# Performance work log

Measured on AMD Instinct MI355X. Metric: run time of the kernel, lower is better.

## Reference

```python
import jax, jax.numpy as jnp
import numpy as np

DIM = 16
N_LAYERS = 3
L = 10
CONST = 1.0
SQRT_XI = 1.0  # np.sqrt(xi) with xi=1
BATCH = 1048576

_TRIL = np.array([(k1, k2) for k1 in range(DIM) for k2 in range(k1)], dtype=np.int32)


def _build_M(Q):
    # scatter Q into strict lower triangle, then symmetrize: M^T + M
    M = jnp.zeros((DIM, DIM), Q.dtype).at[_TRIL[:, 0], _TRIL[:, 1]].set(Q)
    return M.T + M


def setup_inputs() -> dict:
    key = jax.random.key(0)
    k1, k2, k3, k4 = jax.random.split(key, 4)
    return {
        "inputs": jnp.zeros((BATCH, 1), jnp.float32),  # only batch size is used
        "Q": jax.random.uniform(k1, (DIM * (DIM - 1) // 2,), jnp.float32, -0.01, 0.01),
        "delta": jax.random.uniform(k2, (DIM,), jnp.float32, -1.0, 1.0),
        "y0": jax.random.normal(k3, (BATCH, DIM), jnp.float32),
        "vel_noise": jax.random.normal(k4, (N_LAYERS, BATCH, DIM), jnp.float32),
    }


def reference(inputs, Q, delta, y0, vel_noise):
    M = _build_M(Q)

    def force(x):  # gradient of tanh-relaxed Ising energy
        return CONST * (delta + x @ M) * (1.0 - jnp.square(x))

    def leap_step(carry, _):
        y, x, vel = carry
        vel_half = vel + 0.5 * SQRT_XI * force(x)
        y = y + SQRT_XI * vel_half
        x = jnp.tanh(CONST * y)
        vel = vel_half + 0.5 * SQRT_XI * force(x)
        return (y, x, vel), None

    def layer_step(carry, vel0):
        y, x = carry
        (y, x, _), _ = jax.lax.scan(leap_step, (y, x, vel0), None, length=L)
        return (y, x), None

    y = y0
    x = jnp.tanh(CONST * y)
    (y, x), _ = jax.lax.scan(layer_step, (y, x), vel_noise)

    # straight-through estimator: forward = sign (0 -> -1), grad = d tanh
    z = CONST * y
    t = jnp.tanh(z)
    hard = jnp.sign(jnp.sign(z) - 1e-6)
    x_out = jax.lax.stop_gradient(hard - t) + t

    energy = jnp.sum(0.5 * (x_out @ M) * x_out + delta * x_out, axis=-1)
    return x_out, energy
```

## Files before the change

kernel.cpp:

```cpp
#include <hip/hip_runtime.h>
#include <math.h>
#include <stdint.h>

#define DIM 16
#define N_LAYERS 3
#define LSTEPS 10

__global__ void build_M_kernel(const float* __restrict__ Q, float* __restrict__ M) {
    int t = threadIdx.x;
    if (t < DIM * DIM) {
        int i = t >> 4, j = t & (DIM - 1);
        float v = 0.0f;
        if (i != j) {
            int a = i > j ? i : j;
            int c = i > j ? j : i;
            v = Q[(a * (a - 1)) / 2 + c];
        }
        M[t] = v;
    }
}

__device__ __forceinline__ float xla_tanh(float x) {
    #pragma clang fp contract(off)
    float xc = fmaxf(fminf(x, 7.99881172180175781f), -7.99881172180175781f);
    float x2 = xc * xc;
    float p = fmaf(x2, -2.76076847742355e-16f, 2.00018790482477e-13f);
    p = fmaf(x2, p, -8.60467152213735e-11f);
    p = fmaf(x2, p,  5.12229709037114e-08f);
    p = fmaf(x2, p,  1.48572235717979e-05f);
    p = fmaf(x2, p,  6.37261928875436e-04f);
    p = fmaf(x2, p,  4.89352455891786e-03f);
    float num = xc * p;
    float q = fmaf(x2, 1.19825839466702e-06f, 1.18534705686654e-04f);
    q = fmaf(x2, q, 2.26843463243900e-03f);
    q = fmaf(x2, q, 4.89352518554385e-03f);
    float r = num / q;
    return (fabsf(x) < 4e-4f) ? x : r;
}

__global__ __launch_bounds__(256) void ising_kernel(
    const float* __restrict__ M,
    const float* __restrict__ delta,
    const float* __restrict__ y0,
    const float* __restrict__ vnoise,
    float* __restrict__ xout,
    float* __restrict__ eout,
    int batch)
{
    #pragma clang fp contract(off)
    int b = blockIdx.x * blockDim.x + threadIdx.x;
    if (b >= batch) return;

    float y[DIM], x[DIM], vel[DIM], f[DIM];

    {
        const float4* yv = reinterpret_cast<const float4*>(y0 + (size_t)b * DIM);
        #pragma unroll
        for (int q = 0; q < 4; ++q) {
            float4 v = yv[q];
            y[4*q+0] = v.x; y[4*q+1] = v.y; y[4*q+2] = v.z; y[4*q+3] = v.w;
        }
    }

    #pragma unroll
    for (int i = 0; i < DIM; ++i) x[i] = xla_tanh(y[i]);

    #pragma unroll
    for (int i = 0; i < DIM; ++i) {
        float acc = 0.0f;
        #pragma unroll
        for (int k = 0; k < DIM; ++k) acc = fmaf(x[k], M[k*DIM + i], acc);
        float s  = delta[i] + acc;
        float xx = x[i] * x[i];
        float om = 1.0f - xx;
        f[i] = s * om;
    }

    #pragma unroll 1
    for (int l = 0; l < N_LAYERS; ++l) {
        {
            const float4* vv = reinterpret_cast<const float4*>(vnoise + ((size_t)l * batch + b) * DIM);
            #pragma unroll
            for (int q = 0; q < 4; ++q) {
                float4 v = vv[q];
                vel[4*q+0] = v.x; vel[4*q+1] = v.y; vel[4*q+2] = v.z; vel[4*q+3] = v.w;
            }
        }
        #pragma unroll 1
        for (int s = 0; s < LSTEPS; ++s) {
            #pragma unroll
            for (int i = 0; i < DIM; ++i) {
                float hf = 0.5f * f[i];
                float vh = vel[i] + hf;
                y[i] = y[i] + vh;
                vel[i] = vh;
            }
            if (l == N_LAYERS - 1 && s == LSTEPS - 1) break;

            #pragma unroll
            for (int i = 0; i < DIM; ++i) x[i] = xla_tanh(y[i]);

            #pragma unroll
            for (int i = 0; i < DIM; ++i) {
                float acc = 0.0f;
                #pragma unroll
                for (int k = 0; k < DIM; ++k) acc = fmaf(x[k], M[k*DIM + i], acc);
                float sfc = delta[i] + acc;
                float xx  = x[i] * x[i];
                float om  = 1.0f - xx;
                float fi  = sfc * om;
                f[i] = fi;
                float hf = 0.5f * fi;
                vel[i] = vel[i] + hf;
            }
        }
    }

    float xo[DIM];
    #pragma unroll
    for (int i = 0; i < DIM; ++i) {
        float z = y[i];
        float t = xla_tanh(z);
        float s1 = (z > 0.0f) ? 1.0f : ((z < 0.0f) ? -1.0f : 0.0f);
        float s2 = s1 - 1e-6f;
        float hard = (s2 > 0.0f) ? 1.0f : -1.0f;
        float d = hard - t;
        xo[i] = d + t;
    }

    float e = 0.0f;
    #pragma unroll
    for (int i = 0; i < DIM; ++i) {
        float h = 0.0f;
        #pragma unroll
        for (int k = 0; k < DIM; ++k) h = fmaf(xo[k], M[k*DIM + i], h);
        float t1 = 0.5f * h;
        float t2 = t1 * xo[i];
        float t3 = delta[i] * xo[i];
        float el = t2 + t3;
        e = e + el;
    }

    {
        float4* ov = reinterpret_cast<float4*>(xout + (size_t)b * DIM);
        #pragma unroll
        for (int q = 0; q < 4; ++q) {
            float4 v;
            v.x = xo[4*q+0]; v.y = xo[4*q+1]; v.z = xo[4*q+2]; v.w = xo[4*q+3];
            ov[q] = v;
        }
        eout[b] = e;
    }
}

extern "C" void kernel_launch(void* const* d_in, const int* in_sizes, int n_in,
                              void* d_out, int out_size, void* d_ws, size_t ws_size,
                              hipStream_t stream) {
    const float* Q     = (const float*)d_in[1];
    const float* delta = (const float*)d_in[2];
    const float* y0    = (const float*)d_in[3];
    const float* vn    = (const float*)d_in[4];
    int batch = in_sizes[3] / DIM;

    float* M    = (float*)d_ws;
    float* xout = (float*)d_out;
    float* eout = xout + (size_t)batch * DIM;

    build_M_kernel<<<1, 256, 0, stream>>>(Q, M);
    int blocks = (batch + 255) / 256;
    ising_kernel<<<dim3(blocks), dim3(256), 0, stream>>>(M, delta, y0, vn, xout, eout, batch);
}
```

Baseline: 513.0 us.

## Pack math into float2 vectors for packed FMA and use rcp-based division

Rewrites the per-thread leapfrog as 2-wide float vectors so the compiler can emit packed FP32 FMAs/multiplies (v_pk_fma_f32) for the tanh polynomial and the 16x16 matvec, which is reorganised as outer-product accumulation. The IEEE division in tanh becomes a hardware reciprocal plus two Newton refinement FMAs, and the 0.5 factor is folded into the stored force. Together these cut VALU instruction count in a compute-bound kernel. The risks are small last-bit numeric differences from the rcp refinement and higher register pressure from the 8-way vector accumulators.

```diff
diff --git a/kernel.cpp b/kernel.cpp
--- a/kernel.cpp
+++ b/kernel.cpp
@@ -5,6 +5,8 @@
 #define DIM 16
 #define N_LAYERS 3
 #define LSTEPS 10
+
+typedef float v2 __attribute__((ext_vector_type(2)));
 
 __global__ void build_M_kernel(const float* __restrict__ Q, float* __restrict__ M) {
     int t = threadIdx.x;
@@ -20,22 +22,38 @@
     }
 }
 
-__device__ __forceinline__ float xla_tanh(float x) {
+__device__ __forceinline__ v2 rcp2(v2 q) {
+    v2 r;
+    r.x = __builtin_amdgcn_rcpf(q.x);
+    r.y = __builtin_amdgcn_rcpf(q.y);
+    return r;
+}
+
+__device__ __forceinline__ v2 xla_tanh2(v2 xin) {
     #pragma clang fp contract(off)
-    float xc = fmaxf(fminf(x, 7.99881172180175781f), -7.99881172180175781f);
-    float x2 = xc * xc;
-    float p = fmaf(x2, -2.76076847742355e-16f, 2.00018790482477e-13f);
-    p = fmaf(x2, p, -8.60467152213735e-11f);
-    p = fmaf(x2, p,  5.12229709037114e-08f);
-    p = fmaf(x2, p,  1.48572235717979e-05f);
-    p = fmaf(x2, p,  6.37261928875436e-04f);
-    p = fmaf(x2, p,  4.89352455891786e-03f);
-    float num = xc * p;
-    float q = fmaf(x2, 1.19825839466702e-06f, 1.18534705686654e-04f);
-    q = fmaf(x2, q, 2.26843463243900e-03f);
-    q = fmaf(x2, q, 4.89352518554385e-03f);
-    float r = num / q;
-    return (fabsf(x) < 4e-4f) ? x : r;
+    const v2 clampv = (v2)(7.99881172180175781f);
+    v2 xc = __builtin_elementwise_max(__builtin_elementwise_min(xin, clampv), -clampv);
+    v2 x2 = xc * xc;
+    v2 p = __builtin_elementwise_fma(x2, (v2)(-2.76076847742355e-16f), (v2)(2.00018790482477e-13f));
+    p = __builtin_elementwise_fma(x2, p, (v2)(-8.60467152213735e-11f));
+    p = __builtin_elementwise_fma(x2, p, (v2)( 5.12229709037114e-08f));
+    p = __builtin_elementwise_fma(x2, p, (v2)( 1.48572235717979e-05f));
+    p = __builtin_elementwise_fma(x2, p, (v2)( 6.37261928875436e-04f));
+    p = __builtin_elementwise_fma(x2, p, (v2)( 4.89352455891786e-03f));
+    v2 num = xc * p;
+    v2 q = __builtin_elementwise_fma(x2, (v2)(1.19825839466702e-06f), (v2)(1.18534705686654e-04f));
+    q = __builtin_elementwise_fma(x2, q, (v2)(2.26843463243900e-03f));
+    q = __builtin_elementwise_fma(x2, q, (v2)(4.89352518554385e-03f));
+    v2 y0 = rcp2(q);
+    v2 e  = __builtin_elementwise_fma(-q, y0, (v2)(1.0f));
+    v2 y1 = __builtin_elementwise_fma(e, y0, y0);
+    v2 r0 = num * y1;
+    v2 e2 = __builtin_elementwise_fma(-q, r0, num);
+    v2 r  = __builtin_elementwise_fma(e2, y1, r0);
+    v2 out;
+    out.x = (fabsf(xin.x) < 4e-4f) ? xin.x : r.x;
+    out.y = (fabsf(xin.y) < 4e-4f) ? xin.y : r.y;
+    return out;
 }
 
 __global__ __launch_bounds__(256) void ising_kernel(
@@ -51,89 +69,109 @@
     int b = blockIdx.x * blockDim.x + threadIdx.x;
     if (b >= batch) return;
 
-    float y[DIM], x[DIM], vel[DIM], f[DIM];
+    const v2* M2 = reinterpret_cast<const v2*>(M);
+    const v2* d2 = reinterpret_cast<const v2*>(delta);
+
+    v2 y[8], x[8], vel[8], hf[8];
 
     {
-        const float4* yv = reinterpret_cast<const float4*>(y0 + (size_t)b * DIM);
-        #pragma unroll
-        for (int q = 0; q < 4; ++q) {
-            float4 v = yv[q];
-            y[4*q+0] = v.x; y[4*q+1] = v.y; y[4*q+2] = v.z; y[4*q+3] = v.w;
-        }
-    }
-
-    #pragma unroll
-    for (int i = 0; i < DIM; ++i) x[i] = xla_tanh(y[i]);
-
-    #pragma unroll
-    for (int i = 0; i < DIM; ++i) {
-        float acc = 0.0f;
-        #pragma unroll
-        for (int k = 0; k < DIM; ++k) acc = fmaf(x[k], M[k*DIM + i], acc);
-        float s  = delta[i] + acc;
-        float xx = x[i] * x[i];
-        float om = 1.0f - xx;
-        f[i] = s * om;
+        const v2* yv = reinterpret_cast<const v2*>(y0 + (size_t)b * DIM);
+        #pragma unroll
+        for (int ip = 0; ip < 8; ++ip) y[ip] = yv[ip];
+    }
+
+    #pragma unroll
+    for (int ip = 0; ip < 8; ++ip) x[ip] = xla_tanh2(y[ip]);
+
+    #pragma unroll
+    for (int ip = 0; ip < 8; ++ip) hf[ip] = (v2)(0.0f);
+    #pragma unroll
+    for (int k = 0; k < DIM; ++k) {
+        v2 xs = (v2)(x[k >> 1][k & 1]);
+        #pragma unroll
+        for (int ip = 0; ip < 8; ++ip)
+            hf[ip] = __builtin_elementwise_fma(xs, M2[k*8 + ip], hf[ip]);
+    }
+    #pragma unroll
+    for (int ip = 0; ip < 8; ++ip) {
+        v2 s  = d2[ip] + hf[ip];
+        v2 xx = x[ip] * x[ip];
+        v2 om = (v2)(1.0f) - xx;
+        v2 fi = s * om;
+        hf[ip] = (v2)(0.5f) * fi;
     }
 
     #pragma unroll 1
     for (int l = 0; l < N_LAYERS; ++l) {
         {
-            const float4* vv = reinterpret_cast<const float4*>(vnoise + ((size_t)l * batch + b) * DIM);
-            #pragma unroll
-            for (int q = 0; q < 4; ++q) {
-                float4 v = vv[q];
-                vel[4*q+0] = v.x; vel[4*q+1] = v.y; vel[4*q+2] = v.z; vel[4*q+3] = v.w;
-            }
+            const v2* vv = reinterpret_cast<const v2*>(vnoise + ((size_t)l * batch + b) * DIM);
+            #pragma unroll
+            for (int ip = 0; ip < 8; ++ip) vel[ip] = vv[ip];
         }
         #pragma unroll 1
         for (int s = 0; s < LSTEPS; ++s) {
             #pragma unroll
-            for (int i = 0; i < DIM; ++i) {
-                float hf = 0.5f * f[i];
-                float vh = vel[i] + hf;
-                y[i] = y[i] + vh;
-                vel[i] = vh;
+            for (int ip = 0; ip < 8; ++ip) {
+                v2 vh = vel[ip] + hf[ip];
+                y[ip] = y[ip] + vh;
+                vel[ip] = vh;
             }
             if (l == N_LAYERS - 1 && s == LSTEPS - 1) break;
 
             #pragma unroll
-            for (int i = 0; i < DIM; ++i) x[i] = xla_tanh(y[i]);
-
-            #pragma unroll
-            for (int i = 0; i < DIM; ++i) {
-                float acc = 0.0f;
+            for (int ip = 0; ip < 8; ++ip) x[ip] = xla_tanh2(y[ip]);
+
+            v2 acc[8];
+            #pragma unroll
+            for (int ip = 0; ip < 8; ++ip) acc[ip] = (v2)(0.0f);
+            #pragma unroll
+            for (int k = 0; k < DIM; ++k) {
+                v2 xs = (v2)(x[k >> 1][k & 1]);
                 #pragma unroll
-                for (int k = 0; k < DIM; ++k) acc = fmaf(x[k], M[k*DIM + i], acc);
-                float sfc = delta[i] + acc;
-                float xx  = x[i] * x[i];
-                float om  = 1.0f - xx;
-                float fi  = sfc * om;
-                f[i] = fi;
-                float hf = 0.5f * fi;
-                vel[i] = vel[i] + hf;
+                for (int ip = 0; ip < 8; ++ip)
+                    acc[ip] = __builtin_elementwise_fma(xs, M2[k*8 + ip], acc[ip]);
             }
+            #pragma unroll
+            for (int ip = 0; ip < 8; ++ip) {
+                v2 sv = d2[ip] + acc[ip];
+                v2 xx = x[ip] * x[ip];
+                v2 om = (v2)(1.0f) - xx;
+                v2 fi = sv * om;
+                v2 h  = (v2)(0.5f) * fi;
+                hf[ip] = h;
+                vel[ip] = vel[ip] + h;
+            }
         }
     }
 
     float xo[DIM];
     #pragma unroll
+    for (int ip = 0; ip < 8; ++ip) {
+        v2 t2 = xla_tanh2(y[ip]);
+        #pragma unroll
+        for (int h2 = 0; h2 < 2; ++h2) {
+            float z = y[ip][h2];
+            float t = t2[h2];
+            float hard = (z > 0.0f) ? 1.0f : -1.0f;
+            float d = hard - t;
+            xo[2*ip + h2] = d + t;
+        }
+    }
+
+    v2 acc[8];
+    #pragma unroll
+    for (int ip = 0; ip < 8; ++ip) acc[ip] = (v2)(0.0f);
+    #pragma unroll
+    for (int k = 0; k < DIM; ++k) {
+        v2 xs = (v2)(xo[k]);
+        #pragma unroll
+        for (int ip = 0; ip < 8; ++ip)
+            acc[ip] = __builtin_elementwise_fma(xs, M2[k*8 + ip], acc[ip]);
+    }
+    float e = 0.0f;
+    #pragma unroll
     for (int i = 0; i < DIM; ++i) {
-        float z = y[i];
-        float t = xla_tanh(z);
-        float s1 = (z > 0.0f) ? 1.0f : ((z < 0.0f) ? -1.0f : 0.0f);
-        float s2 = s1 - 1e-6f;
-        float hard = (s2 > 0.0f) ? 1.0f : -1.0f;
-        float d = hard - t;
-        xo[i] = d + t;
-    }
-
-    float e = 0.0f;
-    #pragma unroll
-    for (int i = 0; i < DIM; ++i) {
-        float h = 0.0f;
-        #pragma unroll
-        for (int k = 0; k < DIM; ++k) h = fmaf(xo[k], M[k*DIM + i], h);
+        float h  = acc[i >> 1][i & 1];
         float t1 = 0.5f * h;
         float t2 = t1 * xo[i];
         float t3 = delta[i] * xo[i];
@@ -143,12 +181,9 @@
 
     {
         float4* ov = reinterpret_cast<float4*>(xout + (size_t)b * DIM);
-        #pragma unroll
-        for (int q = 0; q < 4; ++q) {
-            float4 v;
-            v.x = xo[4*q+0]; v.y = xo[4*q+1]; v.z = xo[4*q+2]; v.w = xo[4*q+3];
-            ov[q] = v;
-        }
+        const float4* xv = reinterpret_cast<const float4*>(xo);
+        #pragma unroll
+        for (int q = 0; q < 4; ++q) ov[q] = xv[q];
         eout[b] = e;
     }
 }
```

Result: faster. 444.1 us (-13.4%).
